# Kernel tuning notes

Measured on AMD Instinct MI355X. Metric: run time of the kernel, lower is better.

## Reference

```python
import jax, jax.numpy as jnp
import numpy as np

N = 50000      # nodes
E = 800000     # edges per relation
R = 3          # relations
FEAT = 64      # feat_len
HID = 64       # h_dim
NUM_PRED = 5
S = 8192       # seeds


def setup_inputs() -> dict:
    key = jax.random.key(0)
    ks = jax.random.split(key, 24)
    p = lambda k, s: jax.random.normal(k, s, jnp.float32) * 0.05
    x = jax.random.normal(ks[0], (N, FEAT), jnp.float32)
    noise = jax.random.normal(ks[1], (N, HID), jnp.float32)
    seeds = jax.random.randint(ks[2], (S,), 0, N)
    edges = [jax.random.randint(ks[3 + i], (E,), 0, N) for i in range(2 * R)]
    return dict(
        x=x, noise=noise, seeds=seeds,
        src0=edges[0], dst0=edges[1], src1=edges[2], dst1=edges[3],
        src2=edges[4], dst2=edges[5],
        W_conv1=p(ks[9], (R, FEAT, HID)), b_conv1=jnp.zeros((HID,), jnp.float32),
        W_conv2=p(ks[10], (R, HID, HID)), b_conv2=jnp.zeros((HID,), jnp.float32),
        W_lin=p(ks[11], (HID, HID)), b_lin=jnp.zeros((HID,), jnp.float32),
        dW1=p(ks[12], (R, HID, 256)), db1=jnp.zeros((R, 256), jnp.float32),
        dW2=p(ks[13], (R, 256, 32)), db2=jnp.zeros((R, 32), jnp.float32),
        dW3=p(ks[14], (R, 32, 1)), db3=jnp.zeros((R, 1), jnp.float32),
        fW1=p(ks[15], (R, HID, 256)), fb1=jnp.zeros((R, 256), jnp.float32),
        fW2=p(ks[16], (R, 256, 2048)), fb2=jnp.zeros((R, 2048), jnp.float32),
        fW3=p(ks[17], (R, 2048, FEAT * NUM_PRED)), fb3=jnp.zeros((R, FEAT * NUM_PRED), jnp.float32),
    )


def _rel_conv(h, srcs, dsts, W, b):
    # DGL RelGraphConvLayer: per-relation GraphConv(norm='right'), summed over
    # relations (HeteroGraphConv aggregate='sum'), + bias, ReLU (dropout=0).
    out_dim = W.shape[2]
    acc = jnp.zeros((N, out_dim), h.dtype)
    for r in range(R):
        m = (h @ W[r])[srcs[r]]                                   # [E, out]
        agg = jnp.zeros((N, out_dim), h.dtype).at[dsts[r]].add(m)
        deg = jnp.zeros((N,), h.dtype).at[dsts[r]].add(1.0)
        acc = acc + agg / jnp.maximum(deg, 1.0)[:, None]          # norm='right'
    return jax.nn.relu(acc + b)


def reference(x, noise, W_conv1, b_conv1, W_conv2, b_conv2, W_lin, b_lin,
              dW1, db1, dW2, db2, dW3, db3,
              fW1, fb1, fW2, fb2, fW3, fb3,
              seeds, src0, dst0, src1, dst1, src2, dst2):
    srcs = (src0, src1, src2)
    dsts = (dst0, dst1, dst2)
    # two stacked relational conv layers
    h = _rel_conv(x, srcs, dsts, W_conv1, b_conv1)
    h = _rel_conv(h, srcs, dsts, W_conv2, b_conv2)
    # per-ntype Linear + LeakyReLU (dropout=0)
    h = jax.nn.leaky_relu(h @ W_lin + b_lin)
    # Sampler: additive Gaussian noise
    h = h + noise
    # dGen/fGen index inputs[ntype][ind] with ind = enumerate position -> first S rows
    hs = h[:seeds.shape[0]]                                       # [S, HID]
    # ReldGen: per-relation MLP HID->256->32->1 (LeakyReLU, final ReLU)
    z = jax.nn.leaky_relu(jnp.einsum('sd,rdh->rsh', hs, dW1) + db1[:, None, :])
    z = jax.nn.leaky_relu(jnp.einsum('rsh,rhk->rsk', z, dW2) + db2[:, None, :])
    pred_missing = jax.nn.relu(jnp.einsum('rsk,rko->rso', z, dW3) + db3[:, None, :])  # [R,S,1]
    # RelfGen: per-relation MLP HID->256->2048->FEAT*NUM_PRED (ReLU, final Tanh)
    z = jax.nn.relu(jnp.einsum('sd,rdh->rsh', hs, fW1) + fb1[:, None, :])
    z = jax.nn.relu(jnp.einsum('rsh,rhk->rsk', z, fW2) + fb2[:, None, :])
    pred_feat = jnp.tanh(jnp.einsum('rsk,rko->rso', z, fW3) + fb3[:, None, :])        # [R,S,NUM_PRED*FEAT]
    # pack (pred_missing, pred_feat) into one array [R, S, 1 + NUM_PRED*FEAT]
    return jnp.concatenate([pred_missing, pred_feat], axis=-1)
```

## Files before the change

### kernel.cpp

```cpp
#include <hip/hip_runtime.h>
#include <math.h>

#define N_NODES 50000
#define N_EDGES 800000
#define RELS    3
#define HID     64
#define S_SEEDS 8192
#define OUT_COLS 321
#define NB      391
#define BCAP    2560
#define CHUNK   4096
#define NCHUNK  196

typedef __attribute__((ext_vector_type(8))) _Float16 v8h;
typedef __attribute__((ext_vector_type(4))) float v4f;
typedef __attribute__((ext_vector_type(2))) _Float16 h2;

__device__ __forceinline__ unsigned short f32_to_f16(float f) {
    _Float16 h = (_Float16)f;
    return __builtin_bit_cast(unsigned short, h);
}
__device__ __forceinline__ float f16_to_f32(unsigned short u) {
    return (float)__builtin_bit_cast(_Float16, u);
}
__device__ __forceinline__ h2 u2h2(unsigned u) { return __builtin_bit_cast(h2, u); }
__device__ __forceinline__ unsigned h2u(h2 h) { return __builtin_bit_cast(unsigned, h); }

template<int ACT, bool OUT_F16, int BN, int BM = 128>
__global__ __launch_bounds__(256) void gemm_mfma_f16(
    const unsigned short* __restrict__ A, long long sAb, int lda,
    const unsigned short* __restrict__ Bt, long long sBb,
    const float* __restrict__ bias, long long sBiasb,
    void* __restrict__ Cv, long long sCb, int ldc,
    const float* __restrict__ noise,
    int M, int Nc, int K)
{
    constexpr int WC = (BN == 128 || BM == 64) ? 2 : 1;
    constexpr int WR = 4 / WC;
    constexpr int TI = BM / (WR * 16);
    constexpr int TJ = BN / (WC * 16);
    constexpr int TPRA = 256 / BM;
    constexpr int TPRB = 256 / BN;

    __shared__ __align__(16) unsigned short As[2][BM][40];
    __shared__ __align__(16) unsigned short Bs[2][BN][40];

    const int r = blockIdx.z;
    A  += (long long)r * sAb;
    Bt += (long long)r * sBb;
    const float* brow = bias ? bias + (long long)r * sBiasb : nullptr;

    int bx = blockIdx.x, by = blockIdx.y;
    {
        const int nwg  = gridDim.x * gridDim.y;
        const int orig = by * gridDim.x + bx;
        const int q = nwg >> 3, rm = nwg & 7;
        const int xcd = orig & 7, idx = orig >> 3;
        const int wg = (xcd < rm ? xcd * (q + 1) : rm * (q + 1) + (xcd - rm) * q) + idx;
        bx = wg % gridDim.x;
        by = wg / gridDim.x;
    }

    const int tid  = threadIdx.x;
    const int wave = tid >> 6, lane = tid & 63;
    const int quad = lane >> 4, l16 = lane & 15;
    const int wrow = (wave / WC) * (TI * 16);
    const int wcol = (wave % WC) * (TJ * 16);
    const int row0 = by * BM, col0 = bx * BN;

    v4f acc[TI][TJ] = {};

    const int srow = tid / TPRA;
    const int ecol = (tid % TPRA) * (32 / TPRA);
    const int brw  = tid / TPRB;
    const int bcl  = (tid % TPRB) * (32 / TPRB);

    const int gr = row0 + srow;
    const bool aval = (gr < M);
    const unsigned short* aptr = A + (long long)gr * lda + ecol;
    const int gn = col0 + brw;
    const bool bval = (gn < Nc);
    const unsigned short* bptr = Bt + (long long)gn * K + bcl;

    struct Tile { int4 a0, a1, b0, b1; };
    auto loadT = [&](Tile& t, int k0) {
        t.a0 = make_int4(0, 0, 0, 0); t.a1 = make_int4(0, 0, 0, 0);
        t.b0 = make_int4(0, 0, 0, 0); t.b1 = make_int4(0, 0, 0, 0);
        if (aval) {
            t.a0 = *(const int4*)(aptr + k0);
            if constexpr (TPRA == 2) t.a1 = *(const int4*)(aptr + k0 + 8);
        }
        if (bval) {
            t.b0 = *(const int4*)(bptr + k0);
            if constexpr (TPRB == 2) t.b1 = *(const int4*)(bptr + k0 + 8);
        }
    };
    auto storeT = [&](const Tile& t, int buf) {
        *(int4*)(&As[buf][srow][ecol]) = t.a0;
        if constexpr (TPRA == 2) *(int4*)(&As[buf][srow][ecol + 8]) = t.a1;
        *(int4*)(&Bs[buf][brw][bcl]) = t.b0;
        if constexpr (TPRB == 2) *(int4*)(&Bs[buf][brw][bcl + 8]) = t.b1;
    };
    auto compute = [&](int buf) {
        v8h af[TI], bfr[TJ];
#pragma unroll
        for (int i = 0; i < TI; i++)
            af[i] = *(const v8h*)(&As[buf][wrow + i * 16 + l16][quad * 8]);
#pragma unroll
        for (int j = 0; j < TJ; j++)
            bfr[j] = *(const v8h*)(&Bs[buf][wcol + j * 16 + l16][quad * 8]);
#pragma unroll
        for (int i = 0; i < TI; i++)
#pragma unroll
            for (int j = 0; j < TJ; j++)
                acc[i][j] = __builtin_amdgcn_mfma_f32_16x16x32_f16(af[i], bfr[j], acc[i][j], 0, 0, 0);
    };

    const int nt = K >> 5;

    Tile tX, tY;
    loadT(tX, 0);
    storeT(tX, 0);
    if (nt > 1) loadT(tX, 32);
    __syncthreads();

    int cur = 0;
    int t = 0;
    for (; t + 2 < nt; t += 2) {
        loadT(tY, (t + 2) * 32);
        compute(cur);
        storeT(tX, cur ^ 1);
        __syncthreads();
        cur ^= 1;
        if (t + 3 < nt) loadT(tX, (t + 3) * 32);
        compute(cur);
        storeT(tY, cur ^ 1);
        __syncthreads();
        cur ^= 1;
    }
    if (t + 1 < nt) {
        compute(cur);
        storeT(tX, cur ^ 1);
        __syncthreads();
        cur ^= 1;
    }
    compute(cur);

    float* Cf = (float*)Cv + (long long)r * sCb;
    unsigned short* Ch = (unsigned short*)Cv + (long long)r * sCb;
#pragma unroll
    for (int i = 0; i < TI; i++) {
#pragma unroll
        for (int j = 0; j < TJ; j++) {
            int gc = col0 + wcol + j * 16 + l16;
            if (gc >= Nc) continue;
            float bv = brow ? brow[gc] : 0.f;
#pragma unroll
            for (int tt = 0; tt < 4; tt++) {
                int grr = row0 + wrow + i * 16 + quad * 4 + tt;
                if (grr >= M) continue;
                float v = acc[i][j][tt] + bv;
                if (ACT == 1)      v = fmaxf(v, 0.f);
                else if (ACT == 2) v = (v > 0.f) ? v : 0.01f * v;
                else if (ACT == 3) v = tanhf(v);
                if (noise) v += noise[(long long)grr * ldc + gc];
                if (OUT_F16) Ch[(long long)grr * ldc + gc] = f32_to_f16(v);
                else         Cf[(long long)grr * ldc + gc] = v;
            }
        }
    }
}

__global__ __launch_bounds__(512) void fused_f23_kernel(
    const unsigned short* __restrict__ z1,
    const unsigned short* __restrict__ fW2t,
    const float* __restrict__ fb2,
    const unsigned short* __restrict__ fW3t,
    const float* __restrict__ fb3,
    float* __restrict__ out)
{
    __shared__ __align__(16) unsigned short Bs2[64 * 256];
    __shared__ __align__(16) unsigned short Bs3[320 * 64];
    __shared__ __align__(16) unsigned short Z2[128 * 64];
    __shared__ float Fb2[2048];

    int orig = blockIdx.y * gridDim.x + blockIdx.x;
    {
        const int q = (gridDim.x * gridDim.y) >> 3;
        orig = (orig & 7) * q + (orig >> 3);
    }
    const int rel = orig / gridDim.x;
    const int s0  = (orig % gridDim.x) * 128;

    const int tid = threadIdx.x;
    const int wave = tid >> 6;
    const int lane = tid & 63;
    const int quad = lane >> 4, l16 = lane & 15;
    const int wr = wave >> 1;
    const int wc = wave & 1;

    const unsigned short* z1p = z1 + ((long long)rel * S_SEEDS + s0) * 256;
    const unsigned short* w2p = fW2t + (long long)rel * 2048 * 256;
    const unsigned short* w3p = fW3t + (long long)rel * 320 * 2048;

    for (int u = tid; u < 2048; u += 512) Fb2[u] = fb2[rel * 2048 + u];

    v8h zfr[2][8];
#pragma unroll
    for (int i = 0; i < 2; i++) {
        const unsigned short* rp = z1p + (wr * 32 + i * 16 + l16) * 256 + quad * 8;
#pragma unroll
        for (int ks = 0; ks < 8; ks++)
            zfr[i][ks] = *(const v8h*)(rp + ks * 32);
    }

    int4 sr2[4], sr3[5];
    auto stageLoad = [&](int h0) {
#pragma unroll
        for (int u = 0; u < 4; u++) {
            int g = tid + u * 512;
            int row = g >> 5, gc = g & 31;
            sr2[u] = *(const int4*)(w2p + (h0 + row) * 256 + gc * 8);
        }
#pragma unroll
        for (int u = 0; u < 5; u++) {
            int g = tid + u * 512;
            int n = g >> 3, gc = g & 7;
            sr3[u] = *(const int4*)(w3p + (long long)n * 2048 + h0 + gc * 8);
        }
    };
    auto stageWrite = [&]() {
        char* b2 = (char*)Bs2; char* b3 = (char*)Bs3;
#pragma unroll
        for (int u = 0; u < 4; u++) {
            int g = tid + u * 512;
            int row = g >> 5, gc = g & 31;
            *(int4*)(b2 + row * 512 + ((gc * 16) ^ ((row & 7) << 4))) = sr2[u];
        }
#pragma unroll
        for (int u = 0; u < 5; u++) {
            int g = tid + u * 512;
            int n = g >> 3, gc = g & 7;
            *(int4*)(b3 + n * 128 + ((gc * 16) ^ ((n & 7) << 4))) = sr3[u];
        }
    };

    v4f acc3[2][10] = {};

    stageLoad(0);
    stageWrite();
    __syncthreads();

    for (int c = 0; c < 32; c++) {
        const int h0 = c * 64;
        v4f a2[2][2] = {};
        const char* cb2 = (const char*)Bs2;
#pragma unroll
        for (int ks = 0; ks < 8; ks++) {
            v8h bf[2];
#pragma unroll
            for (int j = 0; j < 2; j++) {
                int hl = wc * 32 + j * 16 + l16;
                bf[j] = *(const v8h*)(cb2 + hl * 512 +
                        ((ks * 64 + quad * 16) ^ ((hl & 7) << 4)));
            }
#pragma unroll
            for (int i = 0; i < 2; i++)
#pragma unroll
                for (int j = 0; j < 2; j++)
                    a2[i][j] = __builtin_amdgcn_mfma_f32_16x16x32_f16(zfr[i][ks], bf[j], a2[i][j], 0, 0, 0);
        }
        if (c + 1 < 32) stageLoad(h0 + 64);
        char* zb = (char*)Z2;
#pragma unroll
        for (int i = 0; i < 2; i++)
#pragma unroll
            for (int j = 0; j < 2; j++) {
                int col = wc * 32 + j * 16 + l16;
                float bv = Fb2[h0 + col];
#pragma unroll
                for (int t = 0; t < 4; t++) {
                    int row = wr * 32 + i * 16 + quad * 4 + t;
                    float v = fmaxf(a2[i][j][t] + bv, 0.f);
                    *(unsigned short*)(zb + row * 128 +
                        ((col * 2) ^ ((row & 7) << 4))) = f32_to_f16(v);
                }
            }
        __syncthreads();
#pragma unroll
        for (int ks = 0; ks < 2; ks++) {
            v8h af[2], bf3[10];
#pragma unroll
            for (int i = 0; i < 2; i++) {
                int row = wr * 32 + i * 16 + l16;
                af[i] = *(const v8h*)((const char*)Z2 + row * 128 +
                        ((ks * 64 + quad * 16) ^ ((row & 7) << 4)));
            }
#pragma unroll
            for (int j = 0; j < 10; j++) {
                int n = wc * 160 + j * 16 + l16;
                bf3[j] = *(const v8h*)((const char*)Bs3 + n * 128 +
                        ((ks * 64 + quad * 16) ^ ((n & 7) << 4)));
            }
#pragma unroll
            for (int i = 0; i < 2; i++)
#pragma unroll
                for (int j = 0; j < 10; j++)
                    acc3[i][j] = __builtin_amdgcn_mfma_f32_16x16x32_f16(af[i], bf3[j], acc3[i][j], 0, 0, 0);
        }
        __syncthreads();
        if (c + 1 < 32) {
            stageWrite();
            __syncthreads();
        }
    }

    const float* fb3p = fb3 + rel * 320;
    float* op = out + ((long long)(rel * S_SEEDS + s0)) * OUT_COLS + 1;
#pragma unroll
    for (int i = 0; i < 2; i++)
#pragma unroll
        for (int j = 0; j < 10; j++) {
            int col = wc * 160 + j * 16 + l16;
            float bv = fb3p[col];
#pragma unroll
            for (int t = 0; t < 4; t++) {
                int row = wr * 32 + i * 16 + quad * 4 + t;
                op[(long long)row * OUT_COLS + col] = tanhf(acc3[i][j][t] + bv);
            }
        }
}

__global__ void cvt_f32_f16_kernel(const float* __restrict__ src,
                                   unsigned short* __restrict__ dst, long long n)
{
    long long i = (long long)blockIdx.x * blockDim.x + threadIdx.x;
    if (i < n) dst[i] = f32_to_f16(src[i]);
}

struct TD { const float* s; unsigned short* d; int K, N, nbx, nby, b0; };
struct TDs { TD v[8]; };

__global__ __launch_bounds__(256) void transpose_all_kernel(TDs ds)
{
    __shared__ float t[32][33];
    int b = blockIdx.x;
    int k = 0;
#pragma unroll
    for (int q = 1; q < 8; q++) if (b >= ds.v[q].b0) k = q;
    TD td = ds.v[k];
    int local = b - td.b0;
    int per_r = td.nbx * td.nby;
    int r  = local / per_r;
    int rem = local - r * per_r;
    int by = rem / td.nbx, bx = rem - by * td.nbx;

    const float* src = td.s + (long long)r * td.K * td.N;
    unsigned short* dst = td.d + (long long)r * td.K * td.N;
    int n0 = bx * 32, k0 = by * 32;
    int tx = threadIdx.x & 31, ty = threadIdx.x >> 5;
#pragma unroll
    for (int i = 0; i < 32; i += 8) {
        int kk = k0 + ty + i, n = n0 + tx;
        if (kk < td.K && n < td.N) t[ty + i][tx] = src[(long long)kk * td.N + n];
    }
    __syncthreads();
#pragma unroll
    for (int i = 0; i < 32; i += 8) {
        int n = n0 + ty + i, kk = k0 + tx;
        if (n < td.N && kk < td.K) dst[(long long)n * td.K + kk] = f32_to_f16(t[tx][ty + i]);
    }
}

__global__ __launch_bounds__(256) void bin_fill_kernel(
    const int* __restrict__ s0, const int* __restrict__ d0,
    const int* __restrict__ s1, const int* __restrict__ d1,
    const int* __restrict__ s2, const int* __restrict__ d2,
    int* __restrict__ gcursor,
    unsigned int* __restrict__ bedges)
{
    __shared__ int cnt[NB];
    __shared__ int lstart[NB];
    __shared__ int fillc[NB];
    __shared__ int gstart[NB];
    __shared__ int scan[512];
    __shared__ unsigned int svals[CHUNK];
    __shared__ short sbuck[CHUNK];

    const int rel = blockIdx.y;
    const int* sp = (rel == 0) ? s0 : (rel == 1) ? s1 : s2;
    const int* dp = (rel == 0) ? d0 : (rel == 1) ? d1 : d2;
    const int tid = threadIdx.x;
    const int e0 = blockIdx.x * CHUNK;
    const int n  = min(CHUNK, N_EDGES - e0);

    for (int i = tid; i < NB; i += 256) { cnt[i] = 0; fillc[i] = 0; }
    __syncthreads();

    int myb[CHUNK / 256];
    unsigned int myv[CHUNK / 256];
#pragma unroll
    for (int i = 0; i < CHUNK / 256; i++) {
        int off = tid + i * 256;
        if (off < n) {
            int e = e0 + off;
            int s = sp[e], d = dp[e];
            int b = d >> 7;
            myb[i] = b;
            myv[i] = ((unsigned int)(d & 127) << 16) | (unsigned int)s;
            atomicAdd(&cnt[b], 1);
        } else myb[i] = -1;
    }
    __syncthreads();

    scan[tid]       = (tid < NB) ? cnt[tid] : 0;
    scan[tid + 256] = (tid + 256 < NB) ? cnt[tid + 256] : 0;
    __syncthreads();
    for (int off = 1; off < 512; off <<= 1) {
        int a = (tid >= off) ? scan[tid - off] : 0;
        int b = (tid + 256 >= off) ? scan[tid + 256 - off] : 0;
        __syncthreads();
        scan[tid] += a; scan[tid + 256] += b;
        __syncthreads();
    }
    if (tid < NB)       lstart[tid]       = scan[tid] - cnt[tid];
    if (tid + 256 < NB) lstart[tid + 256] = scan[tid + 256] - cnt[tid + 256];
    __syncthreads();

#pragma unroll
    for (int i = 0; i < CHUNK / 256; i++) {
        int b = myb[i];
        if (b >= 0) {
            int p = lstart[b] + atomicAdd(&fillc[b], 1);
            svals[p] = myv[i];
            sbuck[p] = (short)b;
        }
    }
    if (tid < NB && cnt[tid] > 0)
        gstart[tid] = atomicAdd(&gcursor[rel * NB + tid], cnt[tid]);
    if (tid + 256 < NB && cnt[tid + 256] > 0)
        gstart[tid + 256] = atomicAdd(&gcursor[rel * NB + tid + 256], cnt[tid + 256]);
    __syncthreads();

    for (int p = tid; p < n; p += 256) {
        int b = sbuck[p];
        int pos = gstart[b] + (p - lstart[b]);
        bedges[(long long)(rel * NB + b) * BCAP + pos] = svals[p];
    }
}

__global__ __launch_bounds__(256) void bucket_csr_kernel(
    const unsigned int* __restrict__ bedges,
    const int* __restrict__ gcursor,
    unsigned short* __restrict__ csr16,
    int* __restrict__ browptr)
{
    __shared__ int cnt[128], sc[128], start[128], cur[128];
    __shared__ unsigned short ssorted[BCAP];

    const int id  = blockIdx.y * NB + blockIdx.x;
    const int tid = threadIdx.x;
    const int len = gcursor[id];
    const unsigned int* ep = bedges + (long long)id * BCAP;

    for (int i = tid; i < 128; i += 256) cnt[i] = 0;
    __syncthreads();
    for (int i = tid; i < len; i += 256)
        atomicAdd(&cnt[ep[i] >> 16], 1);
    __syncthreads();

    int v = (tid < 128) ? cnt[tid] : 0;
    if (tid < 128) sc[tid] = v;
    __syncthreads();
    for (int off = 1; off < 128; off <<= 1) {
        int a = (tid < 128 && tid >= off) ? sc[tid - off] : 0;
        __syncthreads();
        if (tid < 128) sc[tid] += a;
        __syncthreads();
    }
    if (tid < 128) { start[tid] = sc[tid] - v; cur[tid] = sc[tid] - v; }
    __syncthreads();

    for (int i = tid; i < len; i += 256) {
        unsigned int vv = ep[i];
        int dl = vv >> 16;
        int pos = atomicAdd(&cur[dl], 1);
        ssorted[pos] = (unsigned short)(vv & 0xFFFFu);
    }
    __syncthreads();

    for (int i = tid; i < len; i += 256)
        csr16[(long long)id * BCAP + i] = ssorted[i];
    if (tid < 128) browptr[id * 128 + tid] = start[tid];
}

__global__ __launch_bounds__(256) void gather_csr_f16_kernel(
    const unsigned short* __restrict__ feat,
    const unsigned short* __restrict__ csr16,
    const int* __restrict__ browptr,
    const int* __restrict__ gcursor,
    unsigned short* __restrict__ agg,
    int M)
{
    int d = (blockIdx.x * 256 + threadIdx.x) >> 6;
    int lane = threadIdx.x & 63;
    if (d >= M) return;
    int bucket = d >> 7, dl = d & 127;
    const int g = lane >> 4;
    const unsigned fo = (unsigned)((lane & 15) << 2);

    int p0[RELS], p1[RELS];
#pragma unroll
    for (int r = 0; r < RELS; r++) {
        int id = r * NB + bucket;
        p0[r] = browptr[id * 128 + dl];
        p1[r] = (dl == 127) ? gcursor[id] : browptr[id * 128 + dl + 1];
    }

    unsigned short* outp = agg + (long long)d * (RELS * HID);

#pragma unroll
    for (int r = 0; r < RELS; r++) {
        const unsigned short* cp = csr16 + (long long)(r * NB + bucket) * BCAP;
        h2 aA01 = (h2)0, aA23 = (h2)0, aB01 = (h2)0, aB23 = (h2)0;
        const int e1 = p1[r];
        int i = p0[r] + g;
        for (; i + 12 < e1; i += 16) {
            unsigned s0 = cp[i], s1 = cp[i + 4], s2 = cp[i + 8], s3 = cp[i + 12];
            uint2 w0 = *(const uint2*)(feat + (s0 << 6) + fo);
            uint2 w1 = *(const uint2*)(feat + (s1 << 6) + fo);
            uint2 w2 = *(const uint2*)(feat + (s2 << 6) + fo);
            uint2 w3 = *(const uint2*)(feat + (s3 << 6) + fo);
            aA01 += u2h2(w0.x) + u2h2(w1.x);
            aA23 += u2h2(w0.y) + u2h2(w1.y);
            aB01 += u2h2(w2.x) + u2h2(w3.x);
            aB23 += u2h2(w2.y) + u2h2(w3.y);
        }
        if (i + 4 < e1) {
            unsigned s0 = cp[i], s1 = cp[i + 4];
            uint2 w0 = *(const uint2*)(feat + (s0 << 6) + fo);
            uint2 w1 = *(const uint2*)(feat + (s1 << 6) + fo);
            aA01 += u2h2(w0.x) + u2h2(w1.x);
            aA23 += u2h2(w0.y) + u2h2(w1.y);
            i += 8;
        }
        if (i < e1) {
            unsigned s0 = cp[i];
            uint2 w0 = *(const uint2*)(feat + (s0 << 6) + fo);
            aB01 += u2h2(w0.x);
            aB23 += u2h2(w0.y);
        }
        h2 a01 = aA01 + aB01, a23 = aA23 + aB23;

        a01 += u2h2((unsigned)__shfl_xor((int)h2u(a01), 16));
        a23 += u2h2((unsigned)__shfl_xor((int)h2u(a23), 16));
        a01 += u2h2((unsigned)__shfl_xor((int)h2u(a01), 32));
        a23 += u2h2((unsigned)__shfl_xor((int)h2u(a23), 32));

        if (lane < 16) {
            float inv = 1.0f / fmaxf((float)(e1 - p0[r]), 1.0f);
            ushort4 o;
            o.x = f32_to_f16((float)a01.x * inv);
            o.y = f32_to_f16((float)a01.y * inv);
            o.z = f32_to_f16((float)a23.x * inv);
            o.w = f32_to_f16((float)a23.y * inv);
            *(ushort4*)(outp + r * HID + fo) = o;
        }
    }
}

__global__ void dhead_kernel(const float* __restrict__ z2d,
                             const float* __restrict__ dW3,
                             const float* __restrict__ db3,
                             float* __restrict__ out)
{
    int idx = blockIdx.x * blockDim.x + threadIdx.x;
    if (idx >= RELS * S_SEEDS) return;
    int r = idx / S_SEEDS;
    const float* zp = z2d + (long long)idx * 32;
    const float* wp = dW3 + r * 32;
    float acc = db3[r];
#pragma unroll
    for (int k = 0; k < 32; k++) acc += zp[k] * wp[k];
    out[(long long)idx * OUT_COLS] = fmaxf(acc, 0.f);
}

extern "C" void kernel_launch(void* const* d_in, const int* in_sizes, int n_in,
                              void* d_out, int out_size, void* d_ws, size_t ws_size,
                              hipStream_t stream)
{
    const float* x     = (const float*)d_in[0];
    const float* noise = (const float*)d_in[1];
    const int* srcs[RELS] = { (const int*)d_in[3], (const int*)d_in[5], (const int*)d_in[7] };
    const int* dsts[RELS] = { (const int*)d_in[4], (const int*)d_in[6], (const int*)d_in[8] };
    const float* Wc1  = (const float*)d_in[9];
    const float* bc1  = (const float*)d_in[10];
    const float* Wc2  = (const float*)d_in[11];
    const float* bc2  = (const float*)d_in[12];
    const float* Wlin = (const float*)d_in[13];
    const float* blin = (const float*)d_in[14];
    const float* dW1  = (const float*)d_in[15];
    const float* db1  = (const float*)d_in[16];
    const float* dW2  = (const float*)d_in[17];
    const float* db2  = (const float*)d_in[18];
    const float* dW3  = (const float*)d_in[19];
    const float* db3  = (const float*)d_in[20];
    const float* fW1  = (const float*)d_in[21];
    const float* fb1  = (const float*)d_in[22];
    const float* fW2  = (const float*)d_in[23];
    const float* fb2  = (const float*)d_in[24];
    const float* fW3  = (const float*)d_in[25];
    const float* fb3  = (const float*)d_in[26];
    float* out = (float*)d_out;
    float* w   = (float*)d_ws;

    int* gcursor = (int*)w;
    int* browptr = (int*)(w + 1280);
    unsigned short* csr16 = (unsigned short*)(w + 151424);
    unsigned short* aggx_hf = (unsigned short*)(w + 1652864);
    unsigned int*   bedges  = (unsigned int*)(w + 1652864 + 2400000);
    float*          z2d     = w + 1652864 + 2400000;
    unsigned short* xhf  = (unsigned short*)(w + 14235776);
    unsigned short* z1hf = (unsigned short*)(w + 14235776);
    unsigned short* h1hf   = (unsigned short*)(w + 17381504);
    unsigned short* agg2hf = (unsigned short*)(w + 18981504);
    unsigned short* h2shf  = (unsigned short*)(w + 19767936);
    unsigned short* hshf   = (unsigned short*)(w + 20030080);
    unsigned short* WcT1   = (unsigned short*)(w + 20292224);
    unsigned short* WcT2   = (unsigned short*)(w + 20298368);
    unsigned short* WlinT  = (unsigned short*)(w + 20304512);
    unsigned short* dW1ht  = (unsigned short*)(w + 20306560);
    unsigned short* dW2ht  = (unsigned short*)(w + 20331136);
    unsigned short* fW1ht  = (unsigned short*)(w + 20343424);
    unsigned short* fW2ht  = (unsigned short*)(w + 20368000);
    unsigned short* fW3ht  = (unsigned short*)(w + 21154432);

    hipMemsetAsync(gcursor, 0, (size_t)RELS * NB * sizeof(int), stream);
    bin_fill_kernel<<<dim3(NCHUNK, RELS), 256, 0, stream>>>(
        srcs[0], dsts[0], srcs[1], dsts[1], srcs[2], dsts[2], gcursor, bedges);
    bucket_csr_kernel<<<dim3(NB, RELS), 256, 0, stream>>>(
        bedges, gcursor, csr16, browptr);

    cvt_f32_f16_kernel<<<(N_NODES * HID + 255) / 256, 256, 0, stream>>>(x, xhf, (long long)N_NODES * HID);
    {
        TDs ds;
        int b0 = 0;
        auto add = [&](int k, const float* s, unsigned short* d, int K, int N, int rels) {
            ds.v[k].s = s; ds.v[k].d = d; ds.v[k].K = K; ds.v[k].N = N;
            ds.v[k].nbx = (N + 31) / 32; ds.v[k].nby = (K + 31) / 32; ds.v[k].b0 = b0;
            b0 += ds.v[k].nbx * ds.v[k].nby * rels;
        };
        add(0, Wc1, WcT1, 192, 64, 1);
        add(1, Wc2, WcT2, 192, 64, 1);
        add(2, Wlin, WlinT, 64, 64, 1);
        add(3, dW1, dW1ht, 64, 256, RELS);
        add(4, dW2, dW2ht, 256, 32, RELS);
        add(5, fW1, fW1ht, 64, 256, RELS);
        add(6, fW2, fW2ht, 256, 2048, RELS);
        add(7, fW3, fW3ht, 2048, 320, RELS);
        transpose_all_kernel<<<b0, 256, 0, stream>>>(ds);
    }

    gather_csr_f16_kernel<<<(N_NODES + 3) / 4, 256, 0, stream>>>(
        xhf, csr16, browptr, gcursor, aggx_hf, N_NODES);
    gemm_mfma_f16<1, true, 64, 64><<<dim3(1, (N_NODES + 63) / 64, 1), 256, 0, stream>>>(
        aggx_hf, 0, RELS * HID, WcT1, 0, bc1, 0,
        h1hf, 0, HID, nullptr, N_NODES, HID, RELS * HID);

    gather_csr_f16_kernel<<<(S_SEEDS + 3) / 4, 256, 0, stream>>>(
        h1hf, csr16, browptr, gcursor, agg2hf, S_SEEDS);
    gemm_mfma_f16<1, true, 64, 64><<<dim3(1, S_SEEDS / 64, 1), 256, 0, stream>>>(
        agg2hf, 0, RELS * HID, WcT2, 0, bc2, 0,
        h2shf, 0, HID, nullptr, S_SEEDS, HID, RELS * HID);

    gemm_mfma_f16<2, true, 64, 64><<<dim3(1, S_SEEDS / 64, 1), 256, 0, stream>>>(
        h2shf, 0, HID, WlinT, 0, blin, 0,
        hshf, 0, HID, noise, S_SEEDS, HID, HID);

    gemm_mfma_f16<2, true, 128><<<dim3(2, S_SEEDS / 128, RELS), 256, 0, stream>>>(
        hshf, 0, HID, dW1ht, 256LL * 64, db1, 256,
        z1hf, (long long)S_SEEDS * 256, 256, nullptr, S_SEEDS, 256, HID);
    gemm_mfma_f16<2, false, 64, 64><<<dim3(1, S_SEEDS / 64, RELS), 256, 0, stream>>>(
        z1hf, (long long)S_SEEDS * 256, 256, dW2ht, 32LL * 256, db2, 32,
        z2d, (long long)S_SEEDS * 32, 32, nullptr, S_SEEDS, 32, 256);
    dhead_kernel<<<(RELS * S_SEEDS + 255) / 256, 256, 0, stream>>>(z2d, dW3, db3, out);

    gemm_mfma_f16<1, true, 128><<<dim3(2, S_SEEDS / 128, RELS), 256, 0, stream>>>(
        hshf, 0, HID, fW1ht, 256LL * 64, fb1, 256,
        z1hf, (long long)S_SEEDS * 256, 256, nullptr, S_SEEDS, 256, HID);
    fused_f23_kernel<<<dim3(S_SEEDS / 128, RELS), 512, 0, stream>>>(
        z1hf, fW2ht, fb2, fW3ht, fb3, out);
}
```

Baseline: 459.8 us.

## Retile fused fGen kernel to 64-row blocks with double-buffered weight staging

New measurement: 715.5 us. +55.6%, slower.

```diff
diff --git a/kernel.cpp b/kernel.cpp
--- a/kernel.cpp
+++ b/kernel.cpp
@@ -179,10 +179,9 @@
     const float* __restrict__ fb3,
     float* __restrict__ out)
 {
-    __shared__ __align__(16) unsigned short Bs2[64 * 256];
-    __shared__ __align__(16) unsigned short Bs3[320 * 64];
-    __shared__ __align__(16) unsigned short Z2[128 * 64];
-    __shared__ float Fb2[2048];
+    __shared__ __align__(16) unsigned short Bs2[2][32 * 256];
+    __shared__ __align__(16) unsigned short Bs3[2][320 * 32];
+    __shared__ __align__(16) unsigned short Z2[64 * 32];
 
     int orig = blockIdx.y * gridDim.x + blockIdx.x;
     {
@@ -190,129 +189,118 @@
         orig = (orig & 7) * q + (orig >> 3);
     }
     const int rel = orig / gridDim.x;
-    const int s0  = (orig % gridDim.x) * 128;
-
-    const int tid = threadIdx.x;
-    const int wave = tid >> 6;
-    const int lane = tid & 63;
+    const int s0  = (orig % gridDim.x) * 64;
+
+    const int tid  = threadIdx.x;
+    const int wave = tid >> 6, lane = tid & 63;
     const int quad = lane >> 4, l16 = lane & 15;
-    const int wr = wave >> 1;
-    const int wc = wave & 1;
+    const int arg = wave >> 1, acg = wave & 1;
+    const int brg = wave >> 2, bcg = wave & 3;
 
     const unsigned short* z1p = z1 + ((long long)rel * S_SEEDS + s0) * 256;
     const unsigned short* w2p = fW2t + (long long)rel * 2048 * 256;
     const unsigned short* w3p = fW3t + (long long)rel * 320 * 2048;
-
-    for (int u = tid; u < 2048; u += 512) Fb2[u] = fb2[rel * 2048 + u];
-
-    v8h zfr[2][8];
-#pragma unroll
-    for (int i = 0; i < 2; i++) {
-        const unsigned short* rp = z1p + (wr * 32 + i * 16 + l16) * 256 + quad * 8;
-#pragma unroll
-        for (int ks = 0; ks < 8; ks++)
-            zfr[i][ks] = *(const v8h*)(rp + ks * 32);
-    }
-
-    int4 sr2[4], sr3[5];
+    const float* fb2p = fb2 + rel * 2048;
+
+    v8h zfr[8];
+    {
+        const unsigned short* rp = z1p + (arg * 16 + l16) * 256 + quad * 8;
+#pragma unroll
+        for (int ks = 0; ks < 8; ks++) zfr[ks] = *(const v8h*)(rp + ks * 32);
+    }
+
+    int4 sr2[2], sr3[3];
     auto stageLoad = [&](int h0) {
 #pragma unroll
-        for (int u = 0; u < 4; u++) {
+        for (int u = 0; u < 2; u++) {
             int g = tid + u * 512;
             int row = g >> 5, gc = g & 31;
             sr2[u] = *(const int4*)(w2p + (h0 + row) * 256 + gc * 8);
         }
 #pragma unroll
-        for (int u = 0; u < 5; u++) {
+        for (int u = 0; u < 3; u++) {
             int g = tid + u * 512;
-            int n = g >> 3, gc = g & 7;
-            sr3[u] = *(const int4*)(w3p + (long long)n * 2048 + h0 + gc * 8);
+            if (u < 2 || tid < 256) {
+                int n = g >> 2, gc = g & 3;
+                sr3[u] = *(const int4*)(w3p + (long long)n * 2048 + h0 + gc * 8);
+            }
         }
     };
-    auto stageWrite = [&]() {
-        char* b2 = (char*)Bs2; char* b3 = (char*)Bs3;
-#pragma unroll
-        for (int u = 0; u < 4; u++) {
+    auto stageWrite = [&](int buf) {
+        char* b2 = (char*)Bs2[buf]; char* b3 = (char*)Bs3[buf];
+#pragma unroll
+        for (int u = 0; u < 2; u++) {
             int g = tid + u * 512;
             int row = g >> 5, gc = g & 31;
             *(int4*)(b2 + row * 512 + ((gc * 16) ^ ((row & 7) << 4))) = sr2[u];
         }
 #pragma unroll
-        for (int u = 0; u < 5; u++) {
+        for (int u = 0; u < 3; u++) {
             int g = tid + u * 512;
-            int n = g >> 3, gc = g & 7;
-            *(int4*)(b3 + n * 128 + ((gc * 16) ^ ((n & 7) << 4))) = sr3[u];
+            if (u < 2 || tid < 256) {
+                int n = g >> 2, gc = g & 3;
+                *(int4*)(b3 + n * 64 + ((gc * 16) ^ ((n & 3) << 4))) = sr3[u];
+            }
         }
     };
 
-    v4f acc3[2][10] = {};
+    v4f acc3[2][5] = {};
 
     stageLoad(0);
-    stageWrite();
-    __syncthreads();
-
-    for (int c = 0; c < 32; c++) {
-        const int h0 = c * 64;
-        v4f a2[2][2] = {};
-        const char* cb2 = (const char*)Bs2;
-#pragma unroll
-        for (int ks = 0; ks < 8; ks++) {
-            v8h bf[2];
-#pragma unroll
-            for (int j = 0; j < 2; j++) {
-                int hl = wc * 32 + j * 16 + l16;
-                bf[j] = *(const v8h*)(cb2 + hl * 512 +
-                        ((ks * 64 + quad * 16) ^ ((hl & 7) << 4)));
+    stageWrite(0);
+    __syncthreads();
+
+    for (int c = 0; c < 64; c++) {
+        const int h0 = c * 32;
+        if (c + 1 < 64) stageLoad(h0 + 32);
+
+        v4f a2 = {};
+        {
+            const char* cb2 = (const char*)Bs2[c & 1];
+            const int hl = acg * 16 + l16;
+            const int hswz = (hl & 7) << 4;
+#pragma unroll
+            for (int ks = 0; ks < 8; ks++) {
+                v8h bf = *(const v8h*)(cb2 + hl * 512 + ((ks * 64 + quad * 16) ^ hswz));
+                a2 = __builtin_amdgcn_mfma_f32_16x16x32_f16(zfr[ks], bf, a2, 0, 0, 0);
+            }
+        }
+        {
+            const int col = acg * 16 + l16;
+            const float bv = fb2p[h0 + col];
+            char* zb = (char*)Z2;
+#pragma unroll
+            for (int t = 0; t < 4; t++) {
+                int row = arg * 16 + quad * 4 + t;
+                float v = fmaxf(a2[t] + bv, 0.f);
+                *(unsigned short*)(zb + row * 64 +
+                    (((col >> 3) ^ (row & 3)) << 4) + (col & 7) * 2) = f32_to_f16(v);
+            }
+        }
+        if (c + 1 < 64) stageWrite((c + 1) & 1);
+        __syncthreads();
+
+        {
+            v8h af[2], bf3[5];
+#pragma unroll
+            for (int i = 0; i < 2; i++) {
+                int row = brg * 32 + i * 16 + l16;
+                af[i] = *(const v8h*)((const char*)Z2 + row * 64 +
+                        ((quad ^ (row & 3)) << 4));
+            }
+            const char* cb3 = (const char*)Bs3[c & 1];
+#pragma unroll
+            for (int j = 0; j < 5; j++) {
+                int n = bcg * 80 + j * 16 + l16;
+                bf3[j] = *(const v8h*)(cb3 + n * 64 + ((quad ^ (n & 3)) << 4));
             }
 #pragma unroll
             for (int i = 0; i < 2; i++)
 #pragma unroll
-                for (int j = 0; j < 2; j++)
-                    a2[i][j] = __builtin_amdgcn_mfma_f32_16x16x32_f16(zfr[i][ks], bf[j], a2[i][j], 0, 0, 0);
-        }
-        if (c + 1 < 32) stageLoad(h0 + 64);
-        char* zb = (char*)Z2;
-#pragma unroll
-        for (int i = 0; i < 2; i++)
-#pragma unroll
-            for (int j = 0; j < 2; j++) {
-                int col = wc * 32 + j * 16 + l16;
-                float bv = Fb2[h0 + col];
-#pragma unroll
-                for (int t = 0; t < 4; t++) {
-                    int row = wr * 32 + i * 16 + quad * 4 + t;
-                    float v = fmaxf(a2[i][j][t] + bv, 0.f);
-                    *(unsigned short*)(zb + row * 128 +
-                        ((col * 2) ^ ((row & 7) << 4))) = f32_to_f16(v);
-                }
-            }
-        __syncthreads();
-#pragma unroll
-        for (int ks = 0; ks < 2; ks++) {
-            v8h af[2], bf3[10];
-#pragma unroll
-            for (int i = 0; i < 2; i++) {
-                int row = wr * 32 + i * 16 + l16;
-                af[i] = *(const v8h*)((const char*)Z2 + row * 128 +
-                        ((ks * 64 + quad * 16) ^ ((row & 7) << 4)));
-            }
-#pragma unroll
-            for (int j = 0; j < 10; j++) {
-                int n = wc * 160 + j * 16 + l16;
-                bf3[j] = *(const v8h*)((const char*)Bs3 + n * 128 +
-                        ((ks * 64 + quad * 16) ^ ((n & 7) << 4)));
-            }
-#pragma unroll
-            for (int i = 0; i < 2; i++)
-#pragma unroll
-                for (int j = 0; j < 10; j++)
+                for (int j = 0; j < 5; j++)
                     acc3[i][j] = __builtin_amdgcn_mfma_f32_16x16x32_f16(af[i], bf3[j], acc3[i][j], 0, 0, 0);
         }
         __syncthreads();
-        if (c + 1 < 32) {
-            stageWrite();
-            __syncthreads();
-        }
     }
 
     const float* fb3p = fb3 + rel * 320;
@@ -320,12 +308,12 @@
 #pragma unroll
     for (int i = 0; i < 2; i++)
 #pragma unroll
-        for (int j = 0; j < 10; j++) {
-            int col = wc * 160 + j * 16 + l16;
+        for (int j = 0; j < 5; j++) {
+            int col = bcg * 80 + j * 16 + l16;
             float bv = fb3p[col];
 #pragma unroll
             for (int t = 0; t < 4; t++) {
-                int row = wr * 32 + i * 16 + quad * 4 + t;
+                int row = brg * 32 + i * 16 + quad * 4 + t;
                 op[(long long)row * OUT_COLS + col] = tanhf(acc3[i][j][t] + bv);
             }
         }
@@ -688,6 +676,6 @@
     gemm_mfma_f16<1, true, 128><<<dim3(2, S_SEEDS / 128, RELS), 256, 0, stream>>>(
         hshf, 0, HID, fW1ht, 256LL * 64, fb1, 256,
         z1hf, (long long)S_SEEDS * 256, 256, nullptr, S_SEEDS, 256, HID);
-    fused_f23_kernel<<<dim3(S_SEEDS / 128, RELS), 512, 0, stream>>>(
+    fused_f23_kernel<<<dim3(S_SEEDS / 64, RELS), 512, 0, stream>>>(
         z1hf, fW2ht, fb2, fW3ht, fb3, out);
 }
```

## Halve fused fGen tile to 64 seeds and remap waves for occupancy

Applied to the files above, without the earlier changes.

After: 780.8 us. 1.7x slower.

```diff
diff --git a/kernel.cpp b/kernel.cpp
--- a/kernel.cpp
+++ b/kernel.cpp
@@ -171,7 +171,7 @@
     }
 }
 
-__global__ __launch_bounds__(512) void fused_f23_kernel(
+__global__ __launch_bounds__(512, 4) void fused_f23_kernel(
     const unsigned short* __restrict__ z1,
     const unsigned short* __restrict__ fW2t,
     const float* __restrict__ fb2,
@@ -181,8 +181,7 @@
 {
     __shared__ __align__(16) unsigned short Bs2[64 * 256];
     __shared__ __align__(16) unsigned short Bs3[320 * 64];
-    __shared__ __align__(16) unsigned short Z2[128 * 64];
-    __shared__ float Fb2[2048];
+    __shared__ __align__(16) unsigned short Z2[64 * 64];
 
     int orig = blockIdx.y * gridDim.x + blockIdx.x;
     {
@@ -190,28 +189,24 @@
         orig = (orig & 7) * q + (orig >> 3);
     }
     const int rel = orig / gridDim.x;
-    const int s0  = (orig % gridDim.x) * 128;
-
-    const int tid = threadIdx.x;
-    const int wave = tid >> 6;
-    const int lane = tid & 63;
+    const int s0  = (orig % gridDim.x) * 64;
+
+    const int tid  = threadIdx.x;
+    const int wave = tid >> 6, lane = tid & 63;
     const int quad = lane >> 4, l16 = lane & 15;
-    const int wr = wave >> 1;
-    const int wc = wave & 1;
+    const int arg = wave >> 1, acg = wave & 1;
+    const int brg = wave >> 2, bcg = wave & 3;
 
     const unsigned short* z1p = z1 + ((long long)rel * S_SEEDS + s0) * 256;
     const unsigned short* w2p = fW2t + (long long)rel * 2048 * 256;
     const unsigned short* w3p = fW3t + (long long)rel * 320 * 2048;
-
-    for (int u = tid; u < 2048; u += 512) Fb2[u] = fb2[rel * 2048 + u];
-
-    v8h zfr[2][8];
-#pragma unroll
-    for (int i = 0; i < 2; i++) {
-        const unsigned short* rp = z1p + (wr * 32 + i * 16 + l16) * 256 + quad * 8;
-#pragma unroll
-        for (int ks = 0; ks < 8; ks++)
-            zfr[i][ks] = *(const v8h*)(rp + ks * 32);
+    const float* fb2p = fb2 + rel * 2048;
+
+    v8h zfr[8];
+    {
+        const unsigned short* rp = z1p + (arg * 16 + l16) * 256 + quad * 8;
+#pragma unroll
+        for (int ks = 0; ks < 8; ks++) zfr[ks] = *(const v8h*)(rp + ks * 32);
     }
 
     int4 sr2[4], sr3[5];
@@ -245,7 +240,7 @@
         }
     };
 
-    v4f acc3[2][10] = {};
+    v4f acc3[2][5] = {};
 
     stageLoad(0);
     stageWrite();
@@ -253,60 +248,62 @@
 
     for (int c = 0; c < 32; c++) {
         const int h0 = c * 64;
-        v4f a2[2][2] = {};
-        const char* cb2 = (const char*)Bs2;
-#pragma unroll
-        for (int ks = 0; ks < 8; ks++) {
-            v8h bf[2];
+        v4f a2[2] = {};
+        {
+            const char* cb2 = (const char*)Bs2;
+#pragma unroll
+            for (int ks = 0; ks < 8; ks++) {
+                v8h bf[2];
+#pragma unroll
+                for (int j = 0; j < 2; j++) {
+                    int hl = acg * 32 + j * 16 + l16;
+                    bf[j] = *(const v8h*)(cb2 + hl * 512 +
+                            ((ks * 64 + quad * 16) ^ ((hl & 7) << 4)));
+                }
+#pragma unroll
+                for (int j = 0; j < 2; j++)
+                    a2[j] = __builtin_amdgcn_mfma_f32_16x16x32_f16(zfr[ks], bf[j], a2[j], 0, 0, 0);
+            }
+        }
+        if (c + 1 < 32) stageLoad(h0 + 64);
+        {
+            char* zb = (char*)Z2;
 #pragma unroll
             for (int j = 0; j < 2; j++) {
-                int hl = wc * 32 + j * 16 + l16;
-                bf[j] = *(const v8h*)(cb2 + hl * 512 +
-                        ((ks * 64 + quad * 16) ^ ((hl & 7) << 4)));
-            }
-#pragma unroll
-            for (int i = 0; i < 2; i++)
-#pragma unroll
-                for (int j = 0; j < 2; j++)
-                    a2[i][j] = __builtin_amdgcn_mfma_f32_16x16x32_f16(zfr[i][ks], bf[j], a2[i][j], 0, 0, 0);
-        }
-        if (c + 1 < 32) stageLoad(h0 + 64);
-        char* zb = (char*)Z2;
-#pragma unroll
-        for (int i = 0; i < 2; i++)
-#pragma unroll
-            for (int j = 0; j < 2; j++) {
-                int col = wc * 32 + j * 16 + l16;
-                float bv = Fb2[h0 + col];
+                int col = acg * 32 + j * 16 + l16;
+                float bv = fb2p[h0 + col];
 #pragma unroll
                 for (int t = 0; t < 4; t++) {
-                    int row = wr * 32 + i * 16 + quad * 4 + t;
-                    float v = fmaxf(a2[i][j][t] + bv, 0.f);
+                    int row = arg * 16 + quad * 4 + t;
+                    float v = fmaxf(a2[j][t] + bv, 0.f);
                     *(unsigned short*)(zb + row * 128 +
                         ((col * 2) ^ ((row & 7) << 4))) = f32_to_f16(v);
                 }
             }
-        __syncthreads();
-#pragma unroll
-        for (int ks = 0; ks < 2; ks++) {
-            v8h af[2], bf3[10];
-#pragma unroll
-            for (int i = 0; i < 2; i++) {
-                int row = wr * 32 + i * 16 + l16;
-                af[i] = *(const v8h*)((const char*)Z2 + row * 128 +
-                        ((ks * 64 + quad * 16) ^ ((row & 7) << 4)));
+        }
+        __syncthreads();
+        {
+#pragma unroll
+            for (int ks = 0; ks < 2; ks++) {
+                v8h af[2], bf3[5];
+#pragma unroll
+                for (int i = 0; i < 2; i++) {
+                    int row = brg * 32 + i * 16 + l16;
+                    af[i] = *(const v8h*)((const char*)Z2 + row * 128 +
+                            ((ks * 64 + quad * 16) ^ ((row & 7) << 4)));
+                }
+#pragma unroll
+                for (int j = 0; j < 5; j++) {
+                    int n = bcg * 80 + j * 16 + l16;
+                    bf3[j] = *(const v8h*)((const char*)Bs3 + n * 128 +
+                            ((ks * 64 + quad * 16) ^ ((n & 7) << 4)));
+                }
+#pragma unroll
+                for (int i = 0; i < 2; i++)
+#pragma unroll
+                    for (int j = 0; j < 5; j++)
+                        acc3[i][j] = __builtin_amdgcn_mfma_f32_16x16x32_f16(af[i], bf3[j], acc3[i][j], 0, 0, 0);
             }
-#pragma unroll
-            for (int j = 0; j < 10; j++) {
-                int n = wc * 160 + j * 16 + l16;
-                bf3[j] = *(const v8h*)((const char*)Bs3 + n * 128 +
-                        ((ks * 64 + quad * 16) ^ ((n & 7) << 4)));
-            }
-#pragma unroll
-            for (int i = 0; i < 2; i++)
-#pragma unroll
-                for (int j = 0; j < 10; j++)
-                    acc3[i][j] = __builtin_amdgcn_mfma_f32_16x16x32_f16(af[i], bf3[j], acc3[i][j], 0, 0, 0);
         }
         __syncthreads();
         if (c + 1 < 32) {
@@ -320,12 +317,12 @@
 #pragma unroll
     for (int i = 0; i < 2; i++)
 #pragma unroll
-        for (int j = 0; j < 10; j++) {
-            int col = wc * 160 + j * 16 + l16;
+        for (int j = 0; j < 5; j++) {
+            int col = bcg * 80 + j * 16 + l16;
             float bv = fb3p[col];
 #pragma unroll
             for (int t = 0; t < 4; t++) {
-                int row = wr * 32 + i * 16 + quad * 4 + t;
+                int row = brg * 32 + i * 16 + quad * 4 + t;
                 op[(long long)row * OUT_COLS + col] = tanhf(acc3[i][j][t] + bv);
             }
         }
@@ -688,6 +685,6 @@
     gemm_mfma_f16<1, true, 128><<<dim3(2, S_SEEDS / 128, RELS), 256, 0, stream>>>(
         hshf, 0, HID, fW1ht, 256LL * 64, fb1, 256,
         z1hf, (long long)S_SEEDS * 256, 256, nullptr, S_SEEDS, 256, HID);
-    fused_f23_kernel<<<dim3(S_SEEDS / 128, RELS), 512, 0, stream>>>(
+    fused_f23_kernel<<<dim3(S_SEEDS / 64, RELS), 512, 0, stream>>>(
         z1hf, fW2ht, fb2, fW3ht, fb3, out);
 }
```
